# Performance work log

Measured on AMD Instinct MI355X. Metric: run time of the kernel, lower is better.

Reference implementation:

```python
import jax, jax.numpy as jnp
import numpy as np
from jax import lax

B, N, D, H, K = 4096, 25, 256, 8, 3  # batch*frames, nodes, d_model, heads, conv kernel


def _layernorm(x, g, b, eps=1e-5):
    mu = jnp.mean(x, axis=-1, keepdims=True)
    var = jnp.var(x, axis=-1, keepdims=True)
    return (x - mu) * lax.rsqrt(var + eps) * g + b


def _conv1d(x_bdn, w):
    # x_bdn: [B, D, N], w: [D_out, D_in, K], padding=K//2 (same as torch Conv1d)
    return lax.conv_general_dilated(x_bdn, w, window_strides=(1,),
                                    padding=[(K // 2, K // 2)],
                                    dimension_numbers=('NCH', 'OIH', 'NCH'))


def setup_inputs() -> dict:
    key = jax.random.key(0)
    ks = jax.random.split(key, 12)
    x = jax.random.normal(ks[0], (B, N, D), dtype=jnp.float32)
    # symmetric adjacency with self-loops (skeleton graph surrogate)
    a = jax.random.bernoulli(ks[1], 0.3, (N, N))
    adj = a | a.T | jnp.eye(N, dtype=bool)
    cs = 1.0 / np.sqrt(D * K)
    wq = jax.random.normal(ks[2], (D, D, K), dtype=jnp.float32) * cs
    wk = jax.random.normal(ks[3], (D, D, K), dtype=jnp.float32) * cs
    wv = jax.random.normal(ks[4], (D, D, K), dtype=jnp.float32) * cs
    gq = jnp.ones((D,), jnp.float32); bq = jnp.zeros((D,), jnp.float32)
    gk = jnp.ones((D,), jnp.float32); bk = jnp.zeros((D,), jnp.float32)
    gv = jnp.ones((D,), jnp.float32); bv = jnp.zeros((D,), jnp.float32)
    rel_table = jax.random.normal(ks[5], (2 * N - 1, H), dtype=jnp.float32) * 0.02
    local_bias = jnp.zeros((H, N, N), jnp.float32)
    wo = jax.random.normal(ks[6], (D, D), dtype=jnp.float32) * (1.0 / np.sqrt(D))
    bo = jnp.zeros((D,), jnp.float32)
    return dict(x=x, adj=adj, wq=wq, wk=wk, wv=wv, gq=gq, bq=bq, gk=gk, bk=bk,
                gv=gv, bv=bv, rel_table=rel_table, local_bias=local_bias, wo=wo, bo=bo)


def reference(x, adj, wq, wk, wv, gq, bq, gk, bk, gv, bv, rel_table, local_bias, wo, bo):
    b, n, d = x.shape
    h = local_bias.shape[0]
    dk = d // h
    xp = x.transpose(0, 2, 1)  # [B, D, N]
    # conv QKV projection over node axis + per-projection LayerNorm + residual
    q = x + _layernorm(_conv1d(xp, wq).transpose(0, 2, 1), gq, bq)
    k = x + _layernorm(_conv1d(xp, wk).transpose(0, 2, 1), gk, bk)
    v = x + _layernorm(_conv1d(xp, wv).transpose(0, 2, 1), gv, bv)
    qh = q.reshape(b, n, h, dk).transpose(0, 2, 1, 3)  # [B, H, N, dk]
    kh = k.reshape(b, n, h, dk).transpose(0, 2, 1, 3)
    vh = v.reshape(b, n, h, dk).transpose(0, 2, 1, 3)
    scores = jnp.einsum('bhnd,bhmd->bhnm', qh, kh) / np.sqrt(dk)
    # relative positional bias over node indices
    coords = jnp.arange(n)
    idx = coords[:, None] - coords[None, :] + n - 1  # [N, N]
    rel = rel_table[idx].transpose(2, 0, 1)  # [H, N, N]
    scores = scores + rel[None] + local_bias[None]
    # adjacency mask (local attention): non-neighbors -> -inf
    scores = jnp.where(adj[None, None], scores, jnp.finfo(scores.dtype).min)
    attn = jax.nn.softmax(scores, axis=-1)
    out = jnp.einsum('bhnm,bhmd->bhnd', attn, vh)  # [B, H, N, dk]
    out = out.transpose(0, 2, 1, 3).reshape(b, n, d)
    return out @ wo.T + bo
```

## Files before the change

kernel.cpp:

```cpp
#include <hip/hip_runtime.h>

#define BB 4096
#define NN 25
#define DD 256
#define HH 8
#define DKH 32
#define MM (BB*NN)

typedef __bf16 bf16;
typedef bf16 bf16x8 __attribute__((ext_vector_type(8)));
typedef bf16 bf16x4 __attribute__((ext_vector_type(4)));
typedef float f32x4 __attribute__((ext_vector_type(4)));
typedef _Float16 h16;
typedef h16 h16x2 __attribute__((ext_vector_type(2)));
typedef h16 h16x4 __attribute__((ext_vector_type(4)));
typedef h16 h16x8 __attribute__((ext_vector_type(8)));

__device__ __forceinline__ void async_load16(const void* g, void* l) {
  __builtin_amdgcn_global_load_lds(
      (const __attribute__((address_space(1))) unsigned int*)g,
      (__attribute__((address_space(3))) unsigned int*)l, 16, 0, 0);
}

#define SCHED_FENCE() __builtin_amdgcn_sched_barrier(0)
#define BARRIER() do { SCHED_FENCE(); __builtin_amdgcn_s_barrier(); SCHED_FENCE(); } while (0)

__global__ __launch_bounds__(256) void k_prep(
    const float* __restrict__ x, bf16* __restrict__ xpad,
    const float* __restrict__ wq, const float* __restrict__ wk, const float* __restrict__ wv,
    const float* __restrict__ rel, const float* __restrict__ lb, const float* __restrict__ wo,
    const void* __restrict__ adj_raw,
    bf16* __restrict__ Wt, h16* __restrict__ woF, float* __restrict__ mb) {
  if (blockIdx.x < 13824) {
    int idx = (blockIdx.x * 256 + threadIdx.x) * 8;
    const int total = BB * 27 * 256;
    if (idx >= total) return;
    int b = idx / (27 * 256);
    int rem = idx - b * 27 * 256;
    int j = rem >> 8;
    int d = rem & 255;
    bf16x8 o;
    if (j >= 1 && j <= 25) {
      const float* src = x + ((b * 25 + (j - 1)) * 256 + d);
      #pragma unroll
      for (int t = 0; t < 8; ++t) o[t] = (bf16)src[t];
    } else {
      #pragma unroll
      for (int t = 0; t < 8; ++t) o[t] = (bf16)0.0f;
    }
    *(bf16x8*)(xpad + idx) = o;
    return;
  }
  const int NWT = 768 * 768;
  const int NMB = HH * NN * 32;
  const int NWF = 8 * 16 * 64 * 8;
  const int total = NWT + NMB + NWF;
  for (int i = (blockIdx.x - 13824) * 256 + threadIdx.x; i < total; i += 512 * 256) {
    if (i < NWT) {
      int j = i / 768, kk = i - j * 768;
      int proj = j >> 8, jo = j & 255;
      int tap = kk >> 8, di = kk & 255;
      const float* w = (proj == 0) ? wq : ((proj == 1) ? wk : wv);
      Wt[i] = (bf16)w[(jo * 256 + di) * 3 + tap];
    } else if (i < NWT + NMB) {
      int t = i - NWT;
      int pair = t >> 5;
      int m = t & 31;
      int h = pair / 25, ii = pair - h * 25;
      float v = -1e30f;
      if (m < 25) {
        const unsigned char* bytes = (const unsigned char*)adj_raw;
        bool u8 = false;
        for (int s = 0; s < 625; ++s) {
          if ((s & 3) && bytes[s]) { u8 = true; break; }
        }
        int amask = u8 ? (bytes[ii * 25 + m] ? 1 : 0)
                       : (((const int*)adj_raw)[ii * 25 + m] ? 1 : 0);
        if (amask)
          v = rel[(ii - m + 24) * HH + h] + lb[h * 625 + ii * 25 + m];
      }
      mb[t] = v;
    } else {
      int e = i - NWT - NMB;
      int c = e & 7, ln = (e >> 3) & 63, nt = (e >> 9) & 15, ks = e >> 13;
      int col = nt * 16 + (ln & 15);
      int k = ks * 32 + (ln >> 4) * 8 + c;
      woF[e] = (h16)wo[col * 256 + k];
    }
  }
}

__global__ __launch_bounds__(512, 2) void k_qkv_gemm8(const bf16* __restrict__ xpad,
                                                      const bf16* __restrict__ Wt,
                                                      bf16* __restrict__ conv) {
  __shared__ bf16 Ab[2][256 * 64];
  __shared__ bf16 Bb[2][256 * 64];

  const int L = blockIdx.x;
  const int sw = (L & 7) * 150 + (L >> 3);
  const int n0 = (sw % 3) * 256;
  const int m0 = (sw / 3) * 256;

  const int tid = threadIdx.x;
  const int lane = tid & 63, wave = tid >> 6;
  const int t16 = lane & 15, quad = lane >> 4;
  const int wr = wave >> 2, wc = wave & 3;

  const int srow = tid >> 3;
  const int sc = ((tid & 7) << 4) ^ ((srow & 7) << 4);
  int aOff[4], bOff[4];
  #pragma unroll
  for (int q = 0; q < 4; ++q) {
    int row = q * 64 + srow;
    int gm = m0 + row;
    int b = gm / 25;
    int n = gm - b * 25;
    aOff[q] = (b * 27 + n) * 512 + sc;
    bOff[q] = (n0 + row) * 1536 + sc;
  }

  const int axr = (t16 & 7) << 3;
  int aoffs[2], boffs[2];
  #pragma unroll
  for (int kk = 0; kk < 2; ++kk) {
    aoffs[kk] = (wr * 128 + t16) * 64 + ((kk * 32 + quad * 8) ^ axr);
    boffs[kk] = (wc * 64 + t16) * 64 + ((kk * 32 + quad * 8) ^ axr);
  }

  f32x4 acc[8][4];
  #pragma unroll
  for (int i = 0; i < 8; ++i)
    #pragma unroll
    for (int j = 0; j < 4; ++j) acc[i][j] = (f32x4){0.f, 0.f, 0.f, 0.f};

  #define ST_B(bufi, tt) do {                                              \
    char* lb_ = (char*)&Bb[bufi][0] + wave * 1024;                         \
    _Pragma("unroll")                                                      \
    for (int q_ = 0; q_ < 4; ++q_)                                         \
      async_load16((const char*)Wt + bOff[q_] + (tt) * 128, lb_ + q_ * 8192); \
  } while (0)
  #define ST_A(bufi, tt) do {                                              \
    char* la_ = (char*)&Ab[bufi][0] + wave * 1024;                         \
    const int ka_ = ((tt) >> 2) * 512 + ((tt) & 3) * 128;                  \
    _Pragma("unroll")                                                      \
    for (int q_ = 0; q_ < 4; ++q_)                                         \
      async_load16((const char*)xpad + aOff[q_] + ka_, la_ + q_ * 8192);   \
  } while (0)

  ST_B(0, 0); ST_A(0, 0);
  ST_B(1, 1); ST_A(1, 1);
  asm volatile("s_waitcnt vmcnt(8)" ::: "memory");
  SCHED_FENCE();
  BARRIER();

  bf16x8 aLo[8], aHi[8], bLo[4], bHi[4];
  {
    const bf16* Ac = &Ab[0][0];
    const bf16* Bc = &Bb[0][0];
    #pragma unroll
    for (int i = 0; i < 4; ++i)
      #pragma unroll
      for (int kk = 0; kk < 2; ++kk)
        aLo[i * 2 + kk] = *(const bf16x8*)(Ac + aoffs[kk] + i * 1024);
    #pragma unroll
    for (int j = 0; j < 2; ++j)
      #pragma unroll
      for (int kk = 0; kk < 2; ++kk)
        bLo[j * 2 + kk] = *(const bf16x8*)(Bc + boffs[kk] + j * 1024);
  }
  SCHED_FENCE();

  for (int u = 0; u < 12; ++u) {
    const int buf = u & 1;
    const bf16* Ac = &Ab[buf][0];
    const bf16* Bc = &Bb[buf][0];
    const bf16* Ac2 = &Ab[buf ^ 1][0];
    const bf16* Bc2 = &Bb[buf ^ 1][0];
    const int st = u + 2;

    #pragma unroll
    for (int j = 0; j < 2; ++j)
      #pragma unroll
      for (int kk = 0; kk < 2; ++kk)
        bHi[j * 2 + kk] = *(const bf16x8*)(Bc + boffs[kk] + (2 + j) * 1024);
    SCHED_FENCE();
    __builtin_amdgcn_s_setprio(1);
    #pragma unroll
    for (int i = 0; i < 4; ++i)
      #pragma unroll
      for (int j = 0; j < 2; ++j)
        #pragma unroll
        for (int kk = 0; kk < 2; ++kk)
          acc[i][j] = __builtin_amdgcn_mfma_f32_16x16x32_bf16(
              aLo[i * 2 + kk], bLo[j * 2 + kk], acc[i][j], 0, 0, 0);
    __builtin_amdgcn_s_setprio(0);
    SCHED_FENCE();

    #pragma unroll
    for (int i = 0; i < 4; ++i)
      #pragma unroll
      for (int kk = 0; kk < 2; ++kk)
        aHi[i * 2 + kk] = *(const bf16x8*)(Ac + aoffs[kk] + (4 + i) * 1024);
    SCHED_FENCE();
    __builtin_amdgcn_s_setprio(1);
    #pragma unroll
    for (int i = 0; i < 4; ++i)
      #pragma unroll
      for (int j = 0; j < 2; ++j)
        #pragma unroll
        for (int kk = 0; kk < 2; ++kk)
          acc[i][2 + j] = __builtin_amdgcn_mfma_f32_16x16x32_bf16(
              aLo[i * 2 + kk], bHi[j * 2 + kk], acc[i][2 + j], 0, 0, 0);
    __builtin_amdgcn_s_setprio(0);
    SCHED_FENCE();

    BARRIER();
    if (st < 12) ST_B(buf, st);
    SCHED_FENCE();
    __builtin_amdgcn_s_setprio(1);
    #pragma unroll
    for (int i = 0; i < 4; ++i)
      #pragma unroll
      for (int j = 0; j < 2; ++j)
        #pragma unroll
        for (int kk = 0; kk < 2; ++kk)
          acc[4 + i][j] = __builtin_amdgcn_mfma_f32_16x16x32_bf16(
              aHi[i * 2 + kk], bLo[j * 2 + kk], acc[4 + i][j], 0, 0, 0);
    __builtin_amdgcn_s_setprio(0);
    SCHED_FENCE();

    if (u < 11) {
      if (u < 10) {
        asm volatile("s_waitcnt vmcnt(4)" ::: "memory");
      } else {
        asm volatile("s_waitcnt vmcnt(0)" ::: "memory");
      }
      SCHED_FENCE();
      BARRIER();
      if (st < 12) ST_A(buf, st);
      #pragma unroll
      for (int i = 0; i < 4; ++i)
        #pragma unroll
        for (int kk = 0; kk < 2; ++kk)
          aLo[i * 2 + kk] = *(const bf16x8*)(Ac2 + aoffs[kk] + i * 1024);
      #pragma unroll
      for (int j = 0; j < 2; ++j)
        #pragma unroll
        for (int kk = 0; kk < 2; ++kk)
          bLo[j * 2 + kk] = *(const bf16x8*)(Bc2 + boffs[kk] + j * 1024);
      SCHED_FENCE();
    }
    __builtin_amdgcn_s_setprio(1);
    #pragma unroll
    for (int i = 0; i < 4; ++i)
      #pragma unroll
      for (int j = 0; j < 2; ++j)
        #pragma unroll
        for (int kk = 0; kk < 2; ++kk)
          acc[4 + i][2 + j] = __builtin_amdgcn_mfma_f32_16x16x32_bf16(
              aHi[i * 2 + kk], bHi[j * 2 + kk], acc[4 + i][2 + j], 0, 0, 0);
    __builtin_amdgcn_s_setprio(0);
    SCHED_FENCE();
  }
  #undef ST_A
  #undef ST_B

  #pragma unroll
  for (int i = 0; i < 8; ++i)
    #pragma unroll
    for (int j = 0; j < 4; ++j) {
      const int col = n0 + wc * 64 + j * 16 + t16;
      #pragma unroll
      for (int r = 0; r < 4; ++r) {
        const int rowm = m0 + wr * 128 + i * 16 + quad * 4 + r;
        conv[(size_t)rowm * 768 + col] = (bf16)acc[i][j][r];
      }
    }
}

__global__ __launch_bounds__(256, 4) void k_attn_oproj(
    const bf16* __restrict__ conv, const float* __restrict__ x,
    const float* __restrict__ gq, const float* __restrict__ bq,
    const float* __restrict__ gk, const float* __restrict__ bk,
    const float* __restrict__ gv, const float* __restrict__ bv,
    const float* __restrict__ mb, const h16* __restrict__ woF,
    const float* __restrict__ bo, float* __restrict__ out) {
  __shared__ bf16 Cs[19456];
  const int b = blockIdx.x;
  const int tid = threadIdx.x;
  const int wave = tid >> 6, lane = tid & 63;

  const char* slab = (const char*)(conv + (size_t)b * 19200);
  for (int c = wave; c < 38; c += 4)
    async_load16(slab + c * 1024 + lane * 16, (char*)Cs + c * 1024);
  asm volatile("s_waitcnt vmcnt(0)" ::: "memory");
  __syncthreads();

  for (int rowi = wave; rowi < 75; rowi += 4) {
    int n = rowi / 3;
    int p = rowi - n * 3;
    const int off = n * 768 + p * 256 + lane * 4;
    bf16x4 cv = *(const bf16x4*)(Cs + off);
    float v0 = (float)cv[0], v1 = (float)cv[1], v2 = (float)cv[2], v3 = (float)cv[3];
    float s = v0 + v1 + v2 + v3;
    float ss = v0 * v0 + v1 * v1 + v2 * v2 + v3 * v3;
    #pragma unroll
    for (int o = 32; o; o >>= 1) {
      s += __shfl_xor(s, o);
      ss += __shfl_xor(ss, o);
    }
    float mu = s * (1.0f / 256.0f);
    float var = ss * (1.0f / 256.0f) - mu * mu;
    float rs = rsqrtf(var + 1e-5f);
    const float* gsel = (p == 0) ? gq : ((p == 1) ? gk : gv);
    const float* bsel = (p == 0) ? bq : ((p == 1) ? bk : bv);
    const int dbase = lane * 4;
    f32x4 gg = *(const f32x4*)(gsel + dbase);
    f32x4 b2 = *(const f32x4*)(bsel + dbase);
    f32x4 xv = *(const f32x4*)(x + ((size_t)(b * 25 + n)) * 256 + dbase);
    h16x4 o;
    o[0] = (h16)((v0 - mu) * rs * gg[0] + b2[0] + xv[0]);
    o[1] = (h16)((v1 - mu) * rs * gg[1] + b2[1] + xv[1]);
    o[2] = (h16)((v2 - mu) * rs * gg[2] + b2[2] + xv[2]);
    o[3] = (h16)((v3 - mu) * rs * gg[3] + b2[3] + xv[3]);
    *(h16x4*)((h16*)Cs + off) = o;
  }
  __syncthreads();

  const h16* Ch = (const h16*)Cs;
  if (tid < HH * NN) {
    const int h = tid / 25;
    const int i = tid - h * 25;

    h16x2 qv[16];
    const h16x2* qp = (const h16x2*)(Ch + i * 768 + h * 32);
    #pragma unroll
    for (int c = 0; c < 16; ++c) qv[c] = qp[c];

    float mrow[28];
    const float* mbp = mb + (h * 25 + i) * 32;
    #pragma unroll
    for (int c = 0; c < 7; ++c) *(f32x4*)(mrow + c * 4) = *(const f32x4*)(mbp + c * 4);

    const float scale = 0.17677669529663687f;
    float sc[25];
    #pragma unroll
    for (int m = 0; m < 25; ++m) {
      const h16x2* kr = (const h16x2*)(Ch + m * 768 + 256 + h * 32);
      float d = 0.f;
      #pragma unroll
      for (int c = 0; c < 16; ++c)
        d = __builtin_amdgcn_fdot2(qv[c], kr[c], d, false);
      sc[m] = d * scale + mrow[m];
    }

    float mx = sc[0];
    #pragma unroll
    for (int m = 1; m < 25; ++m) mx = fmaxf(mx, sc[m]);
    float sum = 0.f;
    #pragma unroll
    for (int m = 0; m < 25; ++m) { sc[m] = __expf(sc[m] - mx); sum += sc[m]; }
    const float inv = 1.0f / sum;

    h16x2 acc[16];
    #pragma unroll
    for (int j = 0; j < 16; ++j) acc[j] = (h16x2){(h16)0.f, (h16)0.f};
    #pragma unroll
    for (int m = 0; m < 25; ++m) {
      h16 w = (h16)(sc[m] * inv);
      h16x2 wp = {w, w};
      const h16x2* vr = (const h16x2*)(Ch + m * 768 + 512 + h * 32);
      #pragma unroll
      for (int j = 0; j < 16; ++j)
        acc[j] = wp * vr[j] + acc[j];
    }

    #pragma unroll
    for (int c = 0; c < 4; ++c) {
      h16x8 o;
      #pragma unroll
      for (int j = 0; j < 4; ++j) {
        o[2 * j]     = acc[c * 4 + j][0];
        o[2 * j + 1] = acc[c * 4 + j][1];
      }
      const int byteoff = i * 1536 + ((h * 64 + c * 16) ^ ((i & 7) << 4));
      *(h16x8*)((char*)Cs + byteoff) = o;
    }
  }
  __syncthreads();

  {
    const int t16 = lane & 15, quad = lane >> 4;
    f32x4 oacc[2][4];
    #pragma unroll
    for (int mt = 0; mt < 2; ++mt)
      #pragma unroll
      for (int jj = 0; jj < 4; ++jj) oacc[mt][jj] = (f32x4){0.f, 0.f, 0.f, 0.f};
    const int arow0 = t16;
    const int arow1 = (16 + t16 > 24) ? 24 : 16 + t16;
    #pragma unroll
    for (int ks = 0; ks < 8; ++ks) {
      h16x8 aF0, aF1;
      {
        const int kb = ks * 64 + quad * 16;
        aF0 = *(const h16x8*)((const char*)Cs + arow0 * 1536 + (kb ^ ((arow0 & 7) << 4)));
        aF1 = *(const h16x8*)((const char*)Cs + arow1 * 1536 + (kb ^ ((arow1 & 7) << 4)));
      }
      #pragma unroll
      for (int jj = 0; jj < 4; ++jj) {
        const h16x8 bF = *(const h16x8*)(woF + ((ks * 16 + wave * 4 + jj) << 9) + lane * 8);
        oacc[0][jj] = __builtin_amdgcn_mfma_f32_16x16x32_f16(aF0, bF, oacc[0][jj], 0, 0, 0);
        oacc[1][jj] = __builtin_amdgcn_mfma_f32_16x16x32_f16(aF1, bF, oacc[1][jj], 0, 0, 0);
      }
    }
    #pragma unroll
    for (int jj = 0; jj < 4; ++jj) {
      const int col = (wave * 4 + jj) * 16 + t16;
      const float bb = bo[col];
      #pragma unroll
      for (int mt = 0; mt < 2; ++mt)
        #pragma unroll
        for (int r = 0; r < 4; ++r) {
          const int row = mt * 16 + quad * 4 + r;
          if (row < 25)
            out[((size_t)b * 25 + row) * 256 + col] = oacc[mt][jj][r] + bb;
        }
    }
  }
}

extern "C" void kernel_launch(void* const* d_in, const int* in_sizes, int n_in,
                              void* d_out, int out_size, void* d_ws, size_t ws_size,
                              hipStream_t stream) {
  (void)in_sizes; (void)n_in; (void)out_size; (void)ws_size;
  const float* x  = (const float*)d_in[0];
  const void*  adj = d_in[1];
  const float* wq = (const float*)d_in[2];
  const float* wk = (const float*)d_in[3];
  const float* wv = (const float*)d_in[4];
  const float* gq = (const float*)d_in[5];
  const float* bq = (const float*)d_in[6];
  const float* gk = (const float*)d_in[7];
  const float* bk = (const float*)d_in[8];
  const float* gv = (const float*)d_in[9];
  const float* bv = (const float*)d_in[10];
  const float* rel = (const float*)d_in[11];
  const float* lb = (const float*)d_in[12];
  const float* wo = (const float*)d_in[13];
  const float* bo = (const float*)d_in[14];
  float* out = (float*)d_out;

  char* ws = (char*)d_ws;
  size_t off = 0;
  auto alloc = [&](size_t bytes) -> void* {
    void* p = ws + off;
    off += (bytes + 255) & ~(size_t)255;
    return p;
  };
  bf16* xpad = (bf16*)alloc((size_t)BB * 27 * 256 * 2);
  bf16* conv = (bf16*)alloc((size_t)MM * 768 * 2);
  bf16* Wt   = (bf16*)alloc((size_t)768 * 768 * 2);
  h16*  woF  = (h16*)alloc((size_t)65536 * 2);
  float* mb  = (float*)alloc((size_t)HH * NN * 32 * 4);

  hipLaunchKernelGGL(k_prep, dim3(14336), dim3(256), 0, stream,
                     x, xpad, wq, wk, wv, rel, lb, wo, adj, Wt, woF, mb);
  hipLaunchKernelGGL(k_qkv_gemm8, dim3(1200), dim3(512), 0, stream, xpad, Wt, conv);
  hipLaunchKernelGGL(k_attn_oproj, dim3(4096), dim3(256), 0, stream,
                     conv, x, gq, bq, gk, bk, gv, bv, mb, woF, bo, out);
}
```

Baseline: 521.6 us.

## Compute per-head attention scores and PV with MFMA instead of scalar dot products

Replaces the per-thread scalar fdot2 attention (200 of 256 threads active) with wave-level 32x32x16 f16 MFMA for both QK^T and PV. Each wave now handles two heads. The mask/bias table is precomputed in the MFMA accumulator layout, and the LayerNorm output is written with an XOR swizzle. Attention output goes to a separate LDS buffer, and occupancy is lowered from 4 to 3 blocks per SM. The aim is to remove the ALU-bound, poorly parallel attention stage, at the cost of extra LDS, cross-lane shuffles and scalar gathers of V.

```diff
diff --git a/kernel.cpp b/kernel.cpp
--- a/kernel.cpp
+++ b/kernel.cpp
@@ -11,6 +11,8 @@
 typedef bf16 bf16x8 __attribute__((ext_vector_type(8)));
 typedef bf16 bf16x4 __attribute__((ext_vector_type(4)));
 typedef float f32x4 __attribute__((ext_vector_type(4)));
+typedef float f32x16 __attribute__((ext_vector_type(16)));
+typedef int   i32x4 __attribute__((ext_vector_type(4)));
 typedef _Float16 h16;
 typedef h16 h16x2 __attribute__((ext_vector_type(2)));
 typedef h16 h16x4 __attribute__((ext_vector_type(4)));
@@ -30,7 +32,7 @@
     const float* __restrict__ wq, const float* __restrict__ wk, const float* __restrict__ wv,
     const float* __restrict__ rel, const float* __restrict__ lb, const float* __restrict__ wo,
     const void* __restrict__ adj_raw,
-    bf16* __restrict__ Wt, h16* __restrict__ woF, float* __restrict__ mb) {
+    bf16* __restrict__ Wt, h16* __restrict__ woF, float* __restrict__ mbF2) {
   if (blockIdx.x < 13824) {
     int idx = (blockIdx.x * 256 + threadIdx.x) * 8;
     const int total = BB * 27 * 256;
@@ -52,7 +54,7 @@
     return;
   }
   const int NWT = 768 * 768;
-  const int NMB = HH * NN * 32;
+  const int NMB = HH * 64 * 16;
   const int NWF = 8 * 16 * 64 * 8;
   const int total = NWT + NMB + NWF;
   for (int i = (blockIdx.x - 13824) * 256 + threadIdx.x; i < total; i += 512 * 256) {
@@ -64,22 +66,27 @@
       Wt[i] = (bf16)w[(jo * 256 + di) * 3 + tap];
     } else if (i < NWT + NMB) {
       int t = i - NWT;
-      int pair = t >> 5;
-      int m = t & 31;
-      int h = pair / 25, ii = pair - h * 25;
-      float v = -1e30f;
-      if (m < 25) {
+      int h = t >> 10;
+      int L = (t >> 4) & 63;
+      int r = t & 15;
+      int iq = L & 31;
+      int m = (r & 3) + 8 * (r >> 2) + 4 * (L >> 5);
+      float v;
+      if (m >= 25) {
+        v = -1e30f;
+      } else if (iq >= 25) {
+        v = 0.0f;
+      } else {
         const unsigned char* bytes = (const unsigned char*)adj_raw;
         bool u8 = false;
         for (int s = 0; s < 625; ++s) {
           if ((s & 3) && bytes[s]) { u8 = true; break; }
         }
-        int amask = u8 ? (bytes[ii * 25 + m] ? 1 : 0)
-                       : (((const int*)adj_raw)[ii * 25 + m] ? 1 : 0);
-        if (amask)
-          v = rel[(ii - m + 24) * HH + h] + lb[h * 625 + ii * 25 + m];
-      }
-      mb[t] = v;
+        int amask = u8 ? (bytes[iq * 25 + m] ? 1 : 0)
+                       : (((const int*)adj_raw)[iq * 25 + m] ? 1 : 0);
+        v = amask ? (rel[(iq - m + 24) * HH + h] + lb[h * 625 + iq * 25 + m]) : -1e30f;
+      }
+      mbF2[t] = v;
     } else {
       int e = i - NWT - NMB;
       int c = e & 7, ln = (e >> 3) & 63, nt = (e >> 9) & 15, ks = e >> 13;
@@ -278,14 +285,15 @@
     }
 }
 
-__global__ __launch_bounds__(256, 4) void k_attn_oproj(
+__global__ __launch_bounds__(256, 3) void k_attn_oproj(
     const bf16* __restrict__ conv, const float* __restrict__ x,
     const float* __restrict__ gq, const float* __restrict__ bq,
     const float* __restrict__ gk, const float* __restrict__ bk,
     const float* __restrict__ gv, const float* __restrict__ bv,
-    const float* __restrict__ mb, const h16* __restrict__ woF,
+    const float* __restrict__ mbF2, const h16* __restrict__ woF,
     const float* __restrict__ bo, float* __restrict__ out) {
   __shared__ bf16 Cs[19456];
+  __shared__ h16 AoS[6400];
   const int b = blockIdx.x;
   const int tid = threadIdx.x;
   const int wave = tid >> 6, lane = tid & 63;
@@ -299,8 +307,8 @@
   for (int rowi = wave; rowi < 75; rowi += 4) {
     int n = rowi / 3;
     int p = rowi - n * 3;
-    const int off = n * 768 + p * 256 + lane * 4;
-    bf16x4 cv = *(const bf16x4*)(Cs + off);
+    const int rbyte = n * 1536 + p * 512 + lane * 8;
+    bf16x4 cv = *(const bf16x4*)((const char*)Cs + rbyte);
     float v0 = (float)cv[0], v1 = (float)cv[1], v2 = (float)cv[2], v3 = (float)cv[3];
     float s = v0 + v1 + v2 + v3;
     float ss = v0 * v0 + v1 * v1 + v2 * v2 + v3 * v3;
@@ -323,68 +331,93 @@
     o[1] = (h16)((v1 - mu) * rs * gg[1] + b2[1] + xv[1]);
     o[2] = (h16)((v2 - mu) * rs * gg[2] + b2[2] + xv[2]);
     o[3] = (h16)((v3 - mu) * rs * gg[3] + b2[3] + xv[3]);
-    *(h16x4*)((h16*)Cs + off) = o;
+    const int wbyte = n * 1536 + ((p * 512 + lane * 8) ^ ((n & 7) << 4));
+    *(h16x4*)((char*)Cs + wbyte) = o;
   }
   __syncthreads();
 
-  const h16* Ch = (const h16*)Cs;
-  if (tid < HH * NN) {
-    const int h = tid / 25;
-    const int i = tid - h * 25;
-
-    h16x2 qv[16];
-    const h16x2* qp = (const h16x2*)(Ch + i * 768 + h * 32);
-    #pragma unroll
-    for (int c = 0; c < 16; ++c) qv[c] = qp[c];
-
-    float mrow[28];
-    const float* mbp = mb + (h * 25 + i) * 32;
-    #pragma unroll
-    for (int c = 0; c < 7; ++c) *(f32x4*)(mrow + c * 4) = *(const f32x4*)(mbp + c * 4);
-
+  {
+    const int hi = lane >> 5;
+    const int dl = lane & 31;
+    const int rowc = dl > 24 ? 24 : dl;
+    const char* base = (const char*)Cs;
     const float scale = 0.17677669529663687f;
-    float sc[25];
-    #pragma unroll
-    for (int m = 0; m < 25; ++m) {
-      const h16x2* kr = (const h16x2*)(Ch + m * 768 + 256 + h * 32);
-      float d = 0.f;
-      #pragma unroll
-      for (int c = 0; c < 16; ++c)
-        d = __builtin_amdgcn_fdot2(qv[c], kr[c], d, false);
-      sc[m] = d * scale + mrow[m];
-    }
-
-    float mx = sc[0];
-    #pragma unroll
-    for (int m = 1; m < 25; ++m) mx = fmaxf(mx, sc[m]);
-    float sum = 0.f;
-    #pragma unroll
-    for (int m = 0; m < 25; ++m) { sc[m] = __expf(sc[m] - mx); sum += sc[m]; }
-    const float inv = 1.0f / sum;
-
-    h16x2 acc[16];
-    #pragma unroll
-    for (int j = 0; j < 16; ++j) acc[j] = (h16x2){(h16)0.f, (h16)0.f};
-    #pragma unroll
-    for (int m = 0; m < 25; ++m) {
-      h16 w = (h16)(sc[m] * inv);
-      h16x2 wp = {w, w};
-      const h16x2* vr = (const h16x2*)(Ch + m * 768 + 512 + h * 32);
-      #pragma unroll
-      for (int j = 0; j < 16; ++j)
-        acc[j] = wp * vr[j] + acc[j];
-    }
-
-    #pragma unroll
-    for (int c = 0; c < 4; ++c) {
-      h16x8 o;
-      #pragma unroll
-      for (int j = 0; j < 4; ++j) {
-        o[2 * j]     = acc[c * 4 + j][0];
-        o[2 * j + 1] = acc[c * 4 + j][1];
-      }
-      const int byteoff = i * 1536 + ((h * 64 + c * 16) ^ ((i & 7) << 4));
-      *(h16x8*)((char*)Cs + byteoff) = o;
+
+    #pragma unroll 1
+    for (int hh = 0; hh < 2; ++hh) {
+      const int h = wave * 2 + hh;
+
+      h16x8 aK[2], bQ[2];
+      #pragma unroll
+      for (int ks = 0; ks < 2; ++ks) {
+        const int kb = h * 64 + ks * 32 + hi * 16;
+        aK[ks] = *(const h16x8*)(base + rowc * 1536 + ((512 + kb) ^ ((rowc & 7) << 4)));
+        bQ[ks] = *(const h16x8*)(base + rowc * 1536 + ((kb) ^ ((rowc & 7) << 4)));
+      }
+      f32x16 sacc = (f32x16)(0.0f);
+      sacc = __builtin_amdgcn_mfma_f32_32x32x16_f16(aK[0], bQ[0], sacc, 0, 0, 0);
+      sacc = __builtin_amdgcn_mfma_f32_32x32x16_f16(aK[1], bQ[1], sacc, 0, 0, 0);
+
+      const float* bp = mbF2 + ((h * 64 + lane) << 4);
+      f32x4 b4[4];
+      #pragma unroll
+      for (int c = 0; c < 4; ++c) b4[c] = *(const f32x4*)(bp + 4 * c);
+      float p[16];
+      #pragma unroll
+      for (int r = 0; r < 16; ++r) p[r] = sacc[r] * scale + b4[r >> 2][r & 3];
+
+      float mx = p[0];
+      #pragma unroll
+      for (int r = 1; r < 16; ++r) mx = fmaxf(mx, p[r]);
+      mx = fmaxf(mx, __shfl_xor(mx, 32));
+      float sum = 0.f;
+      #pragma unroll
+      for (int r = 0; r < 16; ++r) { p[r] = __expf(p[r] - mx); sum += p[r]; }
+      sum += __shfl_xor(sum, 32);
+      const float inv = 1.0f / sum;
+      #pragma unroll
+      for (int r = 0; r < 16; ++r) p[r] *= inv;
+
+      int c8[8], d8[8];
+      #pragma unroll
+      for (int k2 = 0; k2 < 8; ++k2) {
+        h16x2 t;
+        t[0] = (h16)p[2 * k2];
+        t[1] = (h16)p[2 * k2 + 1];
+        c8[k2] = __builtin_bit_cast(int, t);
+      }
+      #pragma unroll
+      for (int k2 = 0; k2 < 8; ++k2) d8[k2] = __shfl_xor(c8[k2], 32);
+      i32x4 f0 = hi ? (i32x4){d8[2], d8[3], c8[2], c8[3]}
+                    : (i32x4){c8[0], c8[1], d8[0], d8[1]};
+      i32x4 f1 = hi ? (i32x4){d8[6], d8[7], c8[6], c8[7]}
+                    : (i32x4){c8[4], c8[5], d8[4], d8[5]};
+      h16x8 fragP0 = __builtin_bit_cast(h16x8, f0);
+      h16x8 fragP1 = __builtin_bit_cast(h16x8, f1);
+
+      h16x8 vb0, vb1;
+      #pragma unroll
+      for (int c = 0; c < 8; ++c) {
+        const int m0v = hi * 8 + c;
+        int m1v = 16 + hi * 8 + c;
+        if (m1v > 24) m1v = 24;
+        const int cb = 1024 + h * 64 + 2 * dl;
+        vb0[c] = *(const h16*)(base + m0v * 1536 + (cb ^ ((m0v & 7) << 4)));
+        vb1[c] = *(const h16*)(base + m1v * 1536 + (cb ^ ((m1v & 7) << 4)));
+      }
+
+      f32x16 oacc = (f32x16)(0.0f);
+      oacc = __builtin_amdgcn_mfma_f32_32x32x16_f16(fragP0, vb0, oacc, 0, 0, 0);
+      oacc = __builtin_amdgcn_mfma_f32_32x32x16_f16(fragP1, vb1, oacc, 0, 0, 0);
+
+      #pragma unroll
+      for (int r = 0; r < 16; ++r) {
+        const int io = (r & 3) + 8 * (r >> 2) + 4 * hi;
+        if (io < 25) {
+          const int wb = io * 512 + ((h * 64 + 2 * dl) ^ ((io & 7) << 4));
+          *(h16*)((char*)AoS + wb) = (h16)oacc[r];
+        }
+      }
     }
   }
   __syncthreads();
@@ -403,8 +436,8 @@
       h16x8 aF0, aF1;
       {
         const int kb = ks * 64 + quad * 16;
-        aF0 = *(const h16x8*)((const char*)Cs + arow0 * 1536 + (kb ^ ((arow0 & 7) << 4)));
-        aF1 = *(const h16x8*)((const char*)Cs + arow1 * 1536 + (kb ^ ((arow1 & 7) << 4)));
+        aF0 = *(const h16x8*)((const char*)AoS + arow0 * 512 + (kb ^ ((arow0 & 7) << 4)));
+        aF1 = *(const h16x8*)((const char*)AoS + arow1 * 512 + (kb ^ ((arow1 & 7) << 4)));
       }
       #pragma unroll
       for (int jj = 0; jj < 4; ++jj) {
@@ -461,11 +494,11 @@
   bf16* conv = (bf16*)alloc((size_t)MM * 768 * 2);
   bf16* Wt   = (bf16*)alloc((size_t)768 * 768 * 2);
   h16*  woF  = (h16*)alloc((size_t)65536 * 2);
-  float* mb  = (float*)alloc((size_t)HH * NN * 32 * 4);
+  float* mbF2 = (float*)alloc((size_t)HH * 64 * 16 * 4);
 
   hipLaunchKernelGGL(k_prep, dim3(14336), dim3(256), 0, stream,
-                     x, xpad, wq, wk, wv, rel, lb, wo, adj, Wt, woF, mb);
+                     x, xpad, wq, wk, wv, rel, lb, wo, adj, Wt, woF, mbF2);
   hipLaunchKernelGGL(k_qkv_gemm8, dim3(1200), dim3(512), 0, stream, xpad, Wt, conv);
   hipLaunchKernelGGL(k_attn_oproj, dim3(4096), dim3(256), 0, stream,
-                     conv, x, gq, bq, gk, bk, gv, bv, mb, woF, bo, out);
+                     conv, x, gq, bq, gk, bk, gv, bv, mbF2, woF, bo, out);
 }
```

Result: no change. 526.2 us (+0.9%).
